# Optimization experiments

Measured on AMD Instinct MI355X. Metric: run time of the kernel, lower is better.

The kernel has to match this reference:

```python
import jax, jax.numpy as jnp
import numpy as np

B, S, D = 2, 2048, 2048
HQ, HKV = 32, 8
DH = D // HQ  # 64
NUM_REP = HQ // HKV  # 4


def setup_inputs() -> dict:
    key = jax.random.key(0)
    k1, k2, k3, k4, k5 = jax.random.split(key, 5)
    scale = 0.02
    return {
        "x": jax.random.normal(k1, (B, S, D), dtype=jnp.float32),
        "Wq": jax.random.normal(k2, (D, HQ * DH), dtype=jnp.float32) * scale,
        "Wk": jax.random.normal(k3, (D, HKV * DH), dtype=jnp.float32) * scale,
        "Wv": jax.random.normal(k4, (D, HKV * DH), dtype=jnp.float32) * scale,
        "Wo": jax.random.normal(k5, (HQ * DH, D), dtype=jnp.float32) * scale,
    }


def reference(x, Wq, Wk, Wv, Wo):
    b, s, _ = x.shape
    # projections
    xq = (x @ Wq).reshape(b, s, HQ, DH)    # [B,S,HQ,DH]
    xk = (x @ Wk).reshape(b, s, HKV, DH)   # [B,S,HKV,DH]
    xv = (x @ Wv).reshape(b, s, HKV, DH)
    # repeat kv heads to match query heads (GQA expand)
    keys = jnp.repeat(xk, NUM_REP, axis=2)    # [B,S,HQ,DH]
    values = jnp.repeat(xv, NUM_REP, axis=2)
    # scores: [B,HQ,S,S], fp32 softmax (no causal mask in original)
    scores = jnp.einsum("bqhd,bkhd->bhqk", xq, keys) / jnp.sqrt(jnp.float32(DH))
    probs = jax.nn.softmax(scores.astype(jnp.float32), axis=-1).astype(xq.dtype)
    context = jnp.einsum("bhqk,bkhd->bqhd", probs, values)  # [B,S,HQ,DH]
    context = context.reshape(b, s, HQ * DH)
    return context @ Wo
```

## Files before the change

kernel.cpp:

```cpp
#include <hip/hip_runtime.h>
#include <cstdint>
#include <cstddef>
#include <cmath>

typedef __bf16 bf16x8 __attribute__((ext_vector_type(8)));
typedef short  s16x4  __attribute__((ext_vector_type(4)));
typedef float  f32x4  __attribute__((ext_vector_type(4)));
typedef unsigned short us4 __attribute__((ext_vector_type(4)));

__device__ __forceinline__ unsigned short f2bf(float f) {
    union { float f; unsigned int u; } v; v.f = f;
    unsigned int u = v.u;
    u += 0x7fffu + ((u >> 16) & 1u);
    return (unsigned short)(u >> 16);
}

__device__ __forceinline__ unsigned int fbits(float f) {
    union { float f; unsigned int u; } v; v.f = f; return v.u;
}

__device__ __forceinline__ unsigned int pk_bf16_trunc(float a, float b) {
    return __builtin_amdgcn_perm(fbits(b), fbits(a), 0x07060302u);
}

__device__ __forceinline__ f32x4 mfma16_bf16(s16x4 a, s16x4 b, f32x4 c) {
    return __builtin_amdgcn_mfma_f32_16x16x16bf16_1k(a, b, c, 0, 0, 0);
}

__device__ __forceinline__ void gld_lds16(const void* g, void* l) {
    __builtin_amdgcn_global_load_lds((__attribute__((address_space(1))) void*)g,
                                     (__attribute__((address_space(3))) void*)l,
                                     16, 0, 0);
}

#define BB   2
#define SS   2048
#define DD   2048
#define HQ   32
#define HKV  8
#define DH   64
#define MM   (BB * SS)
#define NQKV 3072

__global__ __launch_bounds__(256) void cast_f32_bf16(const float* __restrict__ src,
                                                     unsigned short* __restrict__ dst,
                                                     int n) {
    int i = (blockIdx.x * 256 + threadIdx.x) * 4;
    if (i >= n) return;
    const float4 f = *(const float4*)(src + i);
    us4 o;
    o[0] = f2bf(f.x); o[1] = f2bf(f.y); o[2] = f2bf(f.z); o[3] = f2bf(f.w);
    *(us4*)(dst + i) = o;
}

__global__ __launch_bounds__(256) void transpose_cast2(const float* __restrict__ srcA,
                                                       const float* __restrict__ srcB,
                                                       unsigned short* __restrict__ dstA,
                                                       unsigned short* __restrict__ dstB,
                                                       int R, int C) {
    __shared__ __attribute__((aligned(16))) float tile[32][33];
    const float* src = blockIdx.z ? srcB : srcA;
    unsigned short* dst = blockIdx.z ? dstB : dstA;
    const int c0 = blockIdx.x * 32, r0 = blockIdx.y * 32;
    const int tx = threadIdx.x & 31, ty = threadIdx.x >> 5;
    #pragma unroll
    for (int dy = 0; dy < 32; dy += 8)
        tile[ty + dy][tx] = src[(size_t)(r0 + ty + dy) * C + c0 + tx];
    __syncthreads();
    #pragma unroll
    for (int dy = 0; dy < 32; dy += 8)
        dst[(size_t)(c0 + ty + dy) * R + r0 + tx] = f2bf(tile[tx][ty + dy]);
}

__global__ __launch_bounds__(256) void transpose_v(const unsigned short* __restrict__ qkv,
                                                   unsigned short* __restrict__ vt) {
    __shared__ __attribute__((aligned(16))) unsigned short tile[32][33];
    const int s0 = blockIdx.x * 32, d0 = blockIdx.y * 32;
    const int bh = blockIdx.z;
    const int b = bh >> 3, kvh = bh & 7;
    const int tx = threadIdx.x & 31, ty = threadIdx.x >> 5;
    #pragma unroll
    for (int dy = 0; dy < 32; dy += 8)
        tile[ty + dy][tx] =
            qkv[(size_t)(b * SS + s0 + ty + dy) * NQKV + 2560 + kvh * DH + d0 + tx];
    __syncthreads();
    #pragma unroll
    for (int dy = 0; dy < 32; dy += 8)
        vt[(size_t)((b * HKV + kvh) * DH + d0 + ty + dy) * SS + s0 + tx] =
            tile[tx][ty + dy];
}

template <int OUT_BF16>
__global__ __launch_bounds__(256) void gemm_bt(const unsigned short* __restrict__ A,
                                               const unsigned short* __restrict__ Bt,
                                               void* __restrict__ Cout,
                                               int M, int N, int K) {
    __shared__ __attribute__((aligned(16))) unsigned short As[128 * 64];
    __shared__ __attribute__((aligned(16))) unsigned short Bs[128 * 64];
    const int bm = blockIdx.x, bn = blockIdx.y;
    const int tid = threadIdx.x;
    const int wave = tid >> 6, lane = tid & 63;
    const int wm = (wave >> 1) * 64, wn = (wave & 1) * 64;
    const int g = lane >> 4, l15 = lane & 15;
    const int sr = lane >> 3;
    const int sc8 = ((lane & 7) ^ (sr & 7)) * 8;
    const int r7 = l15 & 7;

    f32x4 acc[4][4] = {};
    const unsigned short* aBase = A  + (size_t)(bm * 128) * K;
    const unsigned short* bBase = Bt + (size_t)(bn * 128) * K;

    for (int kt = 0; kt < K; kt += 64) {
        __syncthreads();
        #pragma unroll
        for (int j = 0; j < 4; ++j) {
            const int i = wave * 4 + j;
            gld_lds16(aBase + (size_t)(i * 8 + sr) * K + kt + sc8, &As[i * 512]);
            gld_lds16(bBase + (size_t)(i * 8 + sr) * K + kt + sc8, &Bs[i * 512]);
        }
        __syncthreads();
        #pragma unroll
        for (int ks = 0; ks < 2; ++ks) {
            bf16x8 af[4], bfr[4];
            #pragma unroll
            for (int t = 0; t < 4; ++t) {
                af[t]  = *(const bf16x8*)&As[(wm + t * 16 + l15) * 64 + ((ks * 4 + g) ^ r7) * 8];
                bfr[t] = *(const bf16x8*)&Bs[(wn + t * 16 + l15) * 64 + ((ks * 4 + g) ^ r7) * 8];
            }
            #pragma unroll
            for (int i = 0; i < 4; ++i)
                #pragma unroll
                for (int j = 0; j < 4; ++j)
                    acc[i][j] = __builtin_amdgcn_mfma_f32_16x16x32_bf16(
                        af[i], bfr[j], acc[i][j], 0, 0, 0);
        }
    }
    #pragma unroll
    for (int i = 0; i < 4; ++i) {
        #pragma unroll
        for (int j = 0; j < 4; ++j) {
            const int col = bn * 128 + wn + j * 16 + l15;
            #pragma unroll
            for (int r = 0; r < 4; ++r) {
                const int row = bm * 128 + wm + i * 16 + g * 4 + r;
                const float v = acc[i][j][r];
                if (OUT_BF16)
                    ((unsigned short*)Cout)[(size_t)row * N + col] = f2bf(v);
                else
                    ((float*)Cout)[(size_t)row * N + col] = v;
            }
        }
    }
}

__global__ __launch_bounds__(256, 2) void flash_attn(const unsigned short* __restrict__ qkv,
                                                     const unsigned short* __restrict__ vt,
                                                     unsigned short* __restrict__ ctx) {
    __shared__ __attribute__((aligned(16))) unsigned short Ks[2][64 * 64];
    __shared__ __attribute__((aligned(16))) unsigned short Vs[2][64 * 64];

    const int qt = blockIdx.x, h = blockIdx.y, b = blockIdx.z;
    const int kvh = h >> 2;
    const int tid = threadIdx.x, wave = tid >> 6, lane = tid & 63;
    const int g = lane >> 4, l15 = lane & 15;
    const int sr = lane >> 3;
    const int sc8 = ((lane & 7) ^ (sr & 7)) * 8;
    const int r7 = l15 & 7;
    const int qb = qt * 256 + wave * 64;

    const unsigned short* kbase = qkv + (size_t)(b * SS) * NQKV + 2048 + kvh * DH;
    const unsigned short* vbase = vt + (size_t)((b * HKV + kvh) * DH) * SS;

    bf16x8 qf[4][2];
    #pragma unroll
    for (int n = 0; n < 4; ++n)
        #pragma unroll
        for (int kh = 0; kh < 2; ++kh)
            qf[n][kh] = *(const bf16x8*)(qkv +
                (size_t)(b * SS + qb + n * 16 + l15) * NQKV + h * DH + kh * 32 + g * 8);

    const unsigned short* sp[4];
    size_t sadv;
    if (wave < 2) {
        #pragma unroll
        for (int j = 0; j < 4; ++j)
            sp[j] = kbase + (size_t)((wave * 4 + j) * 8 + sr) * NQKV + sc8;
        sadv = (size_t)64 * NQKV;
    } else {
        #pragma unroll
        for (int j = 0; j < 4; ++j)
            sp[j] = vbase + (size_t)(((wave - 2) * 4 + j) * 8 + sr) * SS + sc8;
        sadv = 64;
    }

    #define STAGE(buf)                                                        \
        do {                                                                  \
            if (wave < 2) {                                                   \
                _Pragma("unroll")                                             \
                for (int j = 0; j < 4; ++j)                                   \
                    gld_lds16(sp[j], &Ks[buf][(wave * 4 + j) * 512]);         \
            } else {                                                          \
                _Pragma("unroll")                                             \
                for (int j = 0; j < 4; ++j)                                   \
                    gld_lds16(sp[j], &Vs[buf][((wave - 2) * 4 + j) * 512]);   \
            }                                                                 \
            _Pragma("unroll")                                                 \
            for (int j = 0; j < 4; ++j) sp[j] += sadv;                        \
        } while (0)

    f32x4 oacc[4][4] = {};
    f32x4 rl4[4] = {};
    const float C2 = 0.18033688011112042f;

    STAGE(0);
    int cur = 0;

    for (int kt = 0; kt < SS; kt += 64) {
        __syncthreads();
        if (kt + 64 < SS) { STAGE(cur ^ 1); }

        const unsigned short* ks = Ks[cur];
        const unsigned short* vs = Vs[cur];

        #pragma unroll
        for (int t = 0; t < 4; ++t) {
            bf16x8 kf0 = *(const bf16x8*)&ks[(t * 16 + l15) * 64 + ((g) ^ r7) * 8];
            bf16x8 kf1 = *(const bf16x8*)&ks[(t * 16 + l15) * 64 + ((4 + g) ^ r7) * 8];
            s16x4 pfr[4];
            #pragma unroll
            for (int n = 0; n < 4; ++n) {
                f32x4 c = {};
                c = __builtin_amdgcn_mfma_f32_16x16x32_bf16(kf0, qf[n][0], c, 0, 0, 0);
                c = __builtin_amdgcn_mfma_f32_16x16x32_bf16(kf1, qf[n][1], c, 0, 0, 0);
                f32x4 e = c * C2 - 8.0f;
                f32x4 p;
                p[0] = __builtin_amdgcn_exp2f(e[0]);
                p[1] = __builtin_amdgcn_exp2f(e[1]);
                p[2] = __builtin_amdgcn_exp2f(e[2]);
                p[3] = __builtin_amdgcn_exp2f(e[3]);
                rl4[n] += p;
                union { uint2 u; s16x4 v; } pk;
                pk.u.x = pk_bf16_trunc(p[0], p[1]);
                pk.u.y = pk_bf16_trunc(p[2], p[3]);
                pfr[n] = pk.v;
            }
            #pragma unroll
            for (int nt = 0; nt < 4; ++nt) {
                const int vrow = nt * 16 + l15;
                s16x4 vf = *(const s16x4*)&vs[vrow * 64 +
                                              ((t * 2 + (g >> 1)) ^ r7) * 8 + (g & 1) * 4];
                #pragma unroll
                for (int m = 0; m < 4; ++m)
                    oacc[m][nt] = mfma16_bf16(pfr[m], vf, oacc[m][nt]);
            }
        }
        cur ^= 1;
    }

    float rl[4];
    #pragma unroll
    for (int n = 0; n < 4; ++n) {
        rl[n] = (rl4[n][0] + rl4[n][1]) + (rl4[n][2] + rl4[n][3]);
        rl[n] += __shfl_xor(rl[n], 16, 64);
        rl[n] += __shfl_xor(rl[n], 32, 64);
    }
    #pragma unroll
    for (int m = 0; m < 4; ++m) {
        #pragma unroll
        for (int r = 0; r < 4; ++r) {
            const float inv = 1.0f / __shfl(rl[m], g * 4 + r, 64);
            const int token = b * SS + qb + m * 16 + g * 4 + r;
            #pragma unroll
            for (int nt = 0; nt < 4; ++nt)
                ctx[(size_t)token * (HQ * DH) + h * DH + nt * 16 + l15] =
                    f2bf(oacc[m][nt][r] * inv);
        }
    }
    #undef STAGE
}

extern "C" void kernel_launch(void* const* d_in, const int* in_sizes, int n_in,
                              void* d_out, int out_size, void* d_ws, size_t ws_size,
                              hipStream_t stream) {
    (void)in_sizes; (void)n_in; (void)out_size; (void)ws_size;
    const float* x  = (const float*)d_in[0];
    const float* Wq = (const float*)d_in[1];
    const float* Wk = (const float*)d_in[2];
    const float* Wv = (const float*)d_in[3];
    const float* Wo = (const float*)d_in[4];
    float* out = (float*)d_out;

    char* ws = (char*)d_ws;
    unsigned short* xb     = (unsigned short*)(ws);
    unsigned short* WqkvT  = (unsigned short*)(ws + 16777216);
    unsigned short* WoT    = (unsigned short*)(ws + 29360128);
    unsigned short* QKV    = (unsigned short*)(ws + 37748736);
    unsigned short* Vt     = (unsigned short*)(ws + 62914560);
    unsigned short* ctx    = (unsigned short*)(ws + 67108864);

    cast_f32_bf16<<<8192, 256, 0, stream>>>(x, xb, MM * DD);
    transpose_cast2<<<dim3(64, 64, 2), 256, 0, stream>>>(Wq, Wo, WqkvT, WoT, 2048, 2048);
    transpose_cast2<<<dim3(16, 64, 2), 256, 0, stream>>>(
        Wk, Wv, WqkvT + (size_t)2048 * 2048, WqkvT + (size_t)2560 * 2048, 2048, 512);

    gemm_bt<1><<<dim3(32, 24), 256, 0, stream>>>(xb, WqkvT, QKV, MM, NQKV, DD);

    transpose_v<<<dim3(64, 2, 16), 256, 0, stream>>>(QKV, Vt);

    flash_attn<<<dim3(8, 32, 2), 256, 0, stream>>>(QKV, Vt, ctx);

    gemm_bt<0><<<dim3(32, 16), 256, 0, stream>>>(ctx, WoT, out, MM, DD, DD);
}
```

Baseline: 318.1 us.

## Use 16x16x32 bf16 MFMA for PV by permuting key row staging order

The PV product now uses the K=32 bf16 MFMA instead of the older 16x16x16 variant, combining two 16-key score tiles into one 8-element A fragment. To make the P fragment layout match the V fragment's k ordering, the K rows are staged into LDS under a bit-permuted key index, so the QK^T output lanes line up with contiguous V columns. This halves the PV MFMA instruction count and widens the V LDS reads to 16 bytes, at the cost of keeping more packed probabilities live in registers.

```diff
diff --git a/kernel.cpp b/kernel.cpp
--- a/kernel.cpp
+++ b/kernel.cpp
@@ -4,7 +4,6 @@
 #include <cmath>
 
 typedef __bf16 bf16x8 __attribute__((ext_vector_type(8)));
-typedef short  s16x4  __attribute__((ext_vector_type(4)));
 typedef float  f32x4  __attribute__((ext_vector_type(4)));
 typedef unsigned short us4 __attribute__((ext_vector_type(4)));
 
@@ -21,10 +20,6 @@
 
 __device__ __forceinline__ unsigned int pk_bf16_trunc(float a, float b) {
     return __builtin_amdgcn_perm(fbits(b), fbits(a), 0x07060302u);
-}
-
-__device__ __forceinline__ f32x4 mfma16_bf16(s16x4 a, s16x4 b, f32x4 c) {
-    return __builtin_amdgcn_mfma_f32_16x16x16bf16_1k(a, b, c, 0, 0, 0);
 }
 
 __device__ __forceinline__ void gld_lds16(const void* g, void* l) {
@@ -183,8 +178,11 @@
     size_t sadv;
     if (wave < 2) {
         #pragma unroll
-        for (int j = 0; j < 4; ++j)
-            sp[j] = kbase + (size_t)((wave * 4 + j) * 8 + sr) * NQKV + sc8;
+        for (int j = 0; j < 4; ++j) {
+            const int rho = (wave * 4 + j) * 8 + sr;
+            const int key = (rho & 0x23) | ((rho & 0x0C) << 1) | ((rho & 0x10) >> 2);
+            sp[j] = kbase + (size_t)key * NQKV + sc8;
+        }
         sadv = (size_t)64 * NQKV;
     } else {
         #pragma unroll
@@ -223,35 +221,41 @@
         const unsigned short* vs = Vs[cur];
 
         #pragma unroll
-        for (int t = 0; t < 4; ++t) {
-            bf16x8 kf0 = *(const bf16x8*)&ks[(t * 16 + l15) * 64 + ((g) ^ r7) * 8];
-            bf16x8 kf1 = *(const bf16x8*)&ks[(t * 16 + l15) * 64 + ((4 + g) ^ r7) * 8];
-            s16x4 pfr[4];
-            #pragma unroll
-            for (int n = 0; n < 4; ++n) {
-                f32x4 c = {};
-                c = __builtin_amdgcn_mfma_f32_16x16x32_bf16(kf0, qf[n][0], c, 0, 0, 0);
-                c = __builtin_amdgcn_mfma_f32_16x16x32_bf16(kf1, qf[n][1], c, 0, 0, 0);
-                f32x4 e = c * C2 - 8.0f;
-                f32x4 p;
-                p[0] = __builtin_amdgcn_exp2f(e[0]);
-                p[1] = __builtin_amdgcn_exp2f(e[1]);
-                p[2] = __builtin_amdgcn_exp2f(e[2]);
-                p[3] = __builtin_amdgcn_exp2f(e[3]);
-                rl4[n] += p;
-                union { uint2 u; s16x4 v; } pk;
-                pk.u.x = pk_bf16_trunc(p[0], p[1]);
-                pk.u.y = pk_bf16_trunc(p[2], p[3]);
-                pfr[n] = pk.v;
+        for (int p = 0; p < 2; ++p) {
+            uint4 pk4[4];
+            #pragma unroll
+            for (int hh = 0; hh < 2; ++hh) {
+                const int t = 2 * p + hh;
+                bf16x8 kf0 = *(const bf16x8*)&ks[(t * 16 + l15) * 64 + ((g) ^ r7) * 8];
+                bf16x8 kf1 = *(const bf16x8*)&ks[(t * 16 + l15) * 64 + ((4 + g) ^ r7) * 8];
+                #pragma unroll
+                for (int n = 0; n < 4; ++n) {
+                    f32x4 c = {};
+                    c = __builtin_amdgcn_mfma_f32_16x16x32_bf16(kf0, qf[n][0], c, 0, 0, 0);
+                    c = __builtin_amdgcn_mfma_f32_16x16x32_bf16(kf1, qf[n][1], c, 0, 0, 0);
+                    f32x4 e = c * C2 - 8.0f;
+                    f32x4 pe;
+                    pe[0] = __builtin_amdgcn_exp2f(e[0]);
+                    pe[1] = __builtin_amdgcn_exp2f(e[1]);
+                    pe[2] = __builtin_amdgcn_exp2f(e[2]);
+                    pe[3] = __builtin_amdgcn_exp2f(e[3]);
+                    rl4[n] += pe;
+                    const unsigned int lo = pk_bf16_trunc(pe[0], pe[1]);
+                    const unsigned int hi = pk_bf16_trunc(pe[2], pe[3]);
+                    if (hh == 0) { pk4[n].x = lo; pk4[n].y = hi; }
+                    else         { pk4[n].z = lo; pk4[n].w = hi; }
+                }
             }
             #pragma unroll
             for (int nt = 0; nt < 4; ++nt) {
-                const int vrow = nt * 16 + l15;
-                s16x4 vf = *(const s16x4*)&vs[vrow * 64 +
-                                              ((t * 2 + (g >> 1)) ^ r7) * 8 + (g & 1) * 4];
+                bf16x8 vf = *(const bf16x8*)&vs[(nt * 16 + l15) * 64 +
+                                                (((p << 2) + g) ^ r7) * 8];
                 #pragma unroll
-                for (int m = 0; m < 4; ++m)
-                    oacc[m][nt] = mfma16_bf16(pfr[m], vf, oacc[m][nt]);
+                for (int m = 0; m < 4; ++m) {
+                    union { uint4 u; bf16x8 v; } pa; pa.u = pk4[m];
+                    oacc[m][nt] = __builtin_amdgcn_mfma_f32_16x16x32_bf16(
+                        pa.v, vf, oacc[m][nt], 0, 0, 0);
+                }
             }
         }
         cur ^= 1;
```

Result: faster. 302.7 us (-4.8%).
